# Kernel tuning notes

Measured on AMD Instinct MI355X. Metric: run time of the kernel, lower is better.

Reference implementation:

```python
import jax, jax.numpy as jnp
import numpy as np

WIN_LEN = 400
WIN_INC = 100
FFT_LEN = 512
EPSILON = float(np.finfo(np.float32).eps)


def _make_kernel():
    # periodic (fftbins=True) hamming window, matching scipy.signal.get_window
    n = np.arange(WIN_LEN)
    window = 0.54 - 0.46 * np.cos(2.0 * np.pi * n / WIN_LEN)
    # direct-DFT basis: rfft of identity, truncated to win_len taps
    fourier_basis = np.fft.rfft(np.eye(FFT_LEN))[:WIN_LEN]          # [win_len, fft_len//2+1]
    kernel = np.concatenate([fourier_basis.real, fourier_basis.imag], axis=1).T  # [2*(fft//2+1), win_len]
    kernel = kernel * window                                        # window applied per tap
    return kernel[:, None, :].astype(np.float32)                    # [514, 1, 400] (OIH)


def setup_inputs() -> dict:
    key = jax.random.key(0)
    inputs = jax.random.normal(key, (16, 160000), dtype=jnp.float32)  # [B, L] waveform
    weight = jnp.asarray(_make_kernel())                              # fixed DFT buffer
    return {"inputs": inputs, "weight": weight}


def reference(inputs, weight):
    pad = WIN_LEN - WIN_INC  # 300
    x = inputs[:, None, :]                                   # [B, 1, L]
    x = jnp.pad(x, ((0, 0), (0, 0), (pad, pad)))             # symmetric pad, as in F.pad
    out = jax.lax.conv_general_dilated(
        x, weight,
        window_strides=(WIN_INC,),
        padding='VALID',
        dimension_numbers=('NCH', 'OIH', 'NCH'),
    )                                                        # [B, 514, T]
    r, i = jnp.split(out, 2, axis=1)                         # real / imag halves [B, 257, T]
    mags = jnp.sqrt(jnp.clip(r * r + i * i, EPSILON))
    phase = jnp.arctan2(i + EPSILON, r + EPSILON)
    return mags, phase
```

## Files before the change

### kernel.cpp

```cpp
#include <hip/hip_runtime.h>
#include <math.h>


#define BATCH 16
#define NSAMP 160000
#define NF 257
#define NT 1603
#define KLEN 400
#define INC 100
#define PADL 300
#define EPSF 1.1920928955078125e-7f
#define TAU 1e-2f

#define FPB 16
#define ZSTR 258
#define XSPAN ((FPB - 1) * INC + KLEN)
#define NTB ((NT + FPB - 1) / FPB)

__device__ __forceinline__ float2 cmul(float2 a, float2 b) {
  return make_float2(a.x * b.x - a.y * b.y, a.x * b.y + a.y * b.x);
}

__device__ __forceinline__ void fft16_dif(float2* a) {
  const float C1 = 0.92387953251128674f;
  const float S1 = 0.38268343236508978f;
  const float R2 = 0.70710678118654752f;
  {
    const float2 W[8] = {{1.f, 0.f},  {C1, -S1},  {R2, -R2},  {S1, -C1},
                         {0.f, -1.f}, {-S1, -C1}, {-R2, -R2}, {-C1, -S1}};
    #pragma unroll
    for (int j = 0; j < 8; ++j) {
      float2 u = a[j], v = a[j + 8];
      a[j] = make_float2(u.x + v.x, u.y + v.y);
      float2 d = make_float2(u.x - v.x, u.y - v.y);
      a[j + 8] = cmul(d, W[j]);
    }
  }
  {
    const float2 W[4] = {{1.f, 0.f}, {R2, -R2}, {0.f, -1.f}, {-R2, -R2}};
    #pragma unroll
    for (int h = 0; h < 16; h += 8)
      #pragma unroll
      for (int j = 0; j < 4; ++j) {
        float2 u = a[h + j], v = a[h + j + 4];
        a[h + j] = make_float2(u.x + v.x, u.y + v.y);
        float2 d = make_float2(u.x - v.x, u.y - v.y);
        a[h + j + 4] = cmul(d, W[j]);
      }
  }
  #pragma unroll
  for (int q = 0; q < 16; q += 4) {
    float2 u0 = a[q], v0 = a[q + 2];
    a[q] = make_float2(u0.x + v0.x, u0.y + v0.y);
    a[q + 2] = make_float2(u0.x - v0.x, u0.y - v0.y);
    float2 u1 = a[q + 1], v1 = a[q + 3];
    a[q + 1] = make_float2(u1.x + v1.x, u1.y + v1.y);
    float2 d = make_float2(u1.x - v1.x, u1.y - v1.y);
    a[q + 3] = make_float2(d.y, -d.x);
  }
  #pragma unroll
  for (int q = 0; q < 16; q += 2) {
    float2 u = a[q], v = a[q + 1];
    a[q] = make_float2(u.x + v.x, u.y + v.y);
    a[q + 1] = make_float2(u.x - v.x, u.y - v.y);
  }
}

__device__ __forceinline__ void emit_fp(float rr, float ii, int ff,
                                        const float* __restrict__ w,
                                        const float* xf,
                                        float* __restrict__ out,
                                        long o, long plane) {
  float ie = ii + EPSF, re = rr + EPSF;
  if (fabsf(ie) < TAU && re < TAU) {
    const float* wr = w + (long)ff * KLEN;
    const float* wi = w + (long)(257 + ff) * KLEN;
    float r2 = 0.f, i2 = 0.f;
    for (int k = 0; k < KLEN; ++k) {
      float xv = xf[k];
      r2 = fmaf(wr[k], xv, r2);
      i2 = fmaf(wi[k], xv, i2);
    }
    rr = r2; ii = i2;
  }
  out[o] = sqrtf(fmaxf(rr * rr + ii * ii, EPSF));
  out[o + plane] = atan2f(ii + EPSF, rr + EPSF);
}

__global__ __launch_bounds__(256, 3)
void stft_fft4(const float* __restrict__ x, const float* __restrict__ w,
               float* __restrict__ out) {
  __shared__ float2 Z[FPB * ZSTR];
  __shared__ float2 tw[132];
  __shared__ float2 tw256[256];
  __shared__ __align__(16) float xs[XSPAN];
  __shared__ __align__(16) float win[KLEN];

  const int tid = threadIdx.x;
  const int t0 = blockIdx.x * FPB;
  const int b = blockIdx.y;
  const int tl = tid & 15;
  const int th = tid >> 4;

  const long xb = (long)b * NSAMP;
  const int base = t0 * INC - PADL;
  for (int r = 0; r < 2; ++r) {
    int i4 = r * 256 + tid;
    if (4 * i4 < XSPAN) {
      int g = base + 4 * i4;
      float4 v;
      if (g >= 0 && g + 3 < NSAMP) {
        v = *(const float4*)(x + xb + g);
      } else {
        v.x = (g + 0 >= 0 && g + 0 < NSAMP) ? x[xb + g + 0] : 0.f;
        v.y = (g + 1 >= 0 && g + 1 < NSAMP) ? x[xb + g + 1] : 0.f;
        v.z = (g + 2 >= 0 && g + 2 < NSAMP) ? x[xb + g + 2] : 0.f;
        v.w = (g + 3 >= 0 && g + 3 < NSAMP) ? x[xb + g + 3] : 0.f;
      }
      *(float4*)&xs[4 * i4] = v;
    }
  }
  if (tid < KLEN / 4) {
    *(float4*)&win[4 * tid] = *(const float4*)(w + 4 * tid);
  }
  {
    double a = (double)tid * (6.283185307179586476925286766559 / 256.0);
    tw256[tid] = make_float2((float)cos(a), (float)(-sin(a)));
  }
  if (tid < 132) {
    double a = (double)tid * (6.283185307179586476925286766559 / 512.0);
    tw[tid] = make_float2((float)cos(a), (float)(-sin(a)));
  }
  __syncthreads();

  float2 a[16];
  const float* xf = &xs[tl * INC];
  #pragma unroll
  for (int n1 = 0; n1 < 12; ++n1) {
    int n = 32 * n1 + 2 * th;
    float2 xv = *(const float2*)&xf[n];
    float2 wv = *(const float2*)&win[n];
    a[n1] = make_float2(xv.x * wv.x, xv.y * wv.y);
  }
  {
    int n = 384 + 2 * th;
    if (n < KLEN) {
      float2 xv = *(const float2*)&xf[n];
      float2 wv = *(const float2*)&win[n];
      a[12] = make_float2(xv.x * wv.x, xv.y * wv.y);
    } else {
      a[12] = make_float2(0.f, 0.f);
    }
  }
  a[13] = a[14] = a[15] = make_float2(0.f, 0.f);

  fft16_dif(a);

  static const int BR[16] = {0, 8, 4, 12, 2, 10, 6, 14,
                             1, 9, 5, 13, 3, 11, 7, 15};
  float2* Zf = Z + tl * ZSTR;
  #pragma unroll
  for (int r = 0; r < 16; ++r) {
    const int k1 = BR[r];
    float2 v = (k1 == 0) ? a[r] : cmul(a[r], tw256[th * k1]);
    Zf[th * 16 + k1] = v;
  }
  __syncthreads();

  float2 g[16];
  #pragma unroll
  for (int n2 = 0; n2 < 16; ++n2) g[n2] = Zf[n2 * 16 + th];
  fft16_dif(g);
  #pragma unroll
  for (int r = 0; r < 16; ++r) {
    const int k2 = BR[r];
    Zf[16 * k2 + th] = g[r];
  }
  __syncthreads();

  const long plane = (long)BATCH * NF * NT;
  const long pb = (long)b * NF * NT;
  for (int r = 0; r < 9; ++r) {
    int tau = r * 256 + tid;
    if (tau < FPB * 129) {
      int t = tau & 15;
      int p = tau >> 4;
      float2* Zt = Z + t * ZSTR;
      float2 z0 = Zt[p];
      float2 z1 = Zt[(256 - p) & 255];
      float2 ze = make_float2(0.5f * (z0.x + z1.x), 0.5f * (z0.y - z1.y));
      float2 zo = make_float2(0.5f * (z0.y + z1.y), 0.5f * (z1.x - z0.x));
      float2 T = tw[p];
      float2 tz = cmul(zo, T);
      float2 ya = make_float2(ze.x + tz.x, ze.y + tz.y);
      float2 yb = make_float2(ze.x - tz.x, tz.y - ze.y);
      int tt = t0 + t;
      if (tt < NT) {
        const float* xfr = &xs[t * INC];
        emit_fp(ya.x, ya.y, p, w, xfr, out, pb + (long)p * NT + tt, plane);
        if (p == 0) {
          emit_fp(yb.x, 0.f, 256, w, xfr, out, pb + (long)256 * NT + tt, plane);
        } else {
          emit_fp(yb.x, yb.y, 256 - p, w, xfr, out,
                  pb + (long)(256 - p) * NT + tt, plane);
        }
      }
    }
  }
}

extern "C" void kernel_launch(void* const* d_in, const int* in_sizes, int n_in,
                              void* d_out, int out_size, void* d_ws, size_t ws_size,
                              hipStream_t stream) {
  const float* x = (const float*)d_in[0];
  const float* w = (const float*)d_in[1];
  float* out = (float*)d_out;

  dim3 grid(NTB, BATCH);
  stft_fft4<<<grid, dim3(256), 0, stream>>>(x, w, out);
}
```

Baseline: 156.0 us.

## Halve FFT scratch LDS via two-pass frame processing and use polynomial atan2

Splits the 16 frames per block into two passes of 8, so the shared FFT scratch buffer shrinks by half. This allows the launch bound to rise from 3 to 5 blocks per SM for higher occupancy. It also replaces atan2f with a minimax polynomial built on a hardware reciprocal, which cuts the cost of the phase computation. The trade-offs are more barriers, half the threads idle during each FFT pass, and a small loss of precision in the phase output.

```diff
diff --git a/kernel.cpp b/kernel.cpp
--- a/kernel.cpp
+++ b/kernel.cpp
@@ -64,6 +64,22 @@
     a[q] = make_float2(u.x + v.x, u.y + v.y);
     a[q + 1] = make_float2(u.x - v.x, u.y - v.y);
   }
+}
+
+__device__ __forceinline__ float fast_atan2(float y, float x) {
+  float ax = fabsf(x), ay = fabsf(y);
+  float mx = fmaxf(ax, ay), mn = fminf(ax, ay);
+  float t = mn * __builtin_amdgcn_rcpf(fmaxf(mx, 1e-37f));
+  float s = t * t;
+  float p = fmaf(s, -0.01172120f, 0.05265332f);
+  p = fmaf(s, p, -0.11643287f);
+  p = fmaf(s, p, 0.19354346f);
+  p = fmaf(s, p, -0.33262347f);
+  p = fmaf(s, p, 0.99997726f);
+  float r = t * p;
+  if (ay > ax) r = 1.57079632679489662f - r;
+  if (x < 0.f) r = 3.14159265358979324f - r;
+  return (y < 0.f) ? -r : r;
 }
 
 __device__ __forceinline__ void emit_fp(float rr, float ii, int ff,
@@ -84,13 +100,13 @@
     rr = r2; ii = i2;
   }
   out[o] = sqrtf(fmaxf(rr * rr + ii * ii, EPSF));
-  out[o + plane] = atan2f(ii + EPSF, rr + EPSF);
-}
-
-__global__ __launch_bounds__(256, 3)
-void stft_fft4(const float* __restrict__ x, const float* __restrict__ w,
+  out[o + plane] = fast_atan2(ii + EPSF, rr + EPSF);
+}
+
+__global__ __launch_bounds__(256, 5)
+void stft_fft5(const float* __restrict__ x, const float* __restrict__ w,
                float* __restrict__ out) {
-  __shared__ float2 Z[FPB * ZSTR];
+  __shared__ float2 Z[8 * ZSTR];
   __shared__ float2 tw[132];
   __shared__ float2 tw256[256];
   __shared__ __align__(16) float xs[XSPAN];
@@ -158,54 +174,65 @@
 
   static const int BR[16] = {0, 8, 4, 12, 2, 10, 6, 14,
                              1, 9, 5, 13, 3, 11, 7, 15};
-  float2* Zf = Z + tl * ZSTR;
-  #pragma unroll
-  for (int r = 0; r < 16; ++r) {
-    const int k1 = BR[r];
-    float2 v = (k1 == 0) ? a[r] : cmul(a[r], tw256[th * k1]);
-    Zf[th * 16 + k1] = v;
-  }
-  __syncthreads();
-
-  float2 g[16];
-  #pragma unroll
-  for (int n2 = 0; n2 < 16; ++n2) g[n2] = Zf[n2 * 16 + th];
-  fft16_dif(g);
-  #pragma unroll
-  for (int r = 0; r < 16; ++r) {
-    const int k2 = BR[r];
-    Zf[16 * k2 + th] = g[r];
-  }
-  __syncthreads();
-
   const long plane = (long)BATCH * NF * NT;
   const long pb = (long)b * NF * NT;
-  for (int r = 0; r < 9; ++r) {
-    int tau = r * 256 + tid;
-    if (tau < FPB * 129) {
-      int t = tau & 15;
-      int p = tau >> 4;
-      float2* Zt = Z + t * ZSTR;
-      float2 z0 = Zt[p];
-      float2 z1 = Zt[(256 - p) & 255];
-      float2 ze = make_float2(0.5f * (z0.x + z1.x), 0.5f * (z0.y - z1.y));
-      float2 zo = make_float2(0.5f * (z0.y + z1.y), 0.5f * (z1.x - z0.x));
-      float2 T = tw[p];
-      float2 tz = cmul(zo, T);
-      float2 ya = make_float2(ze.x + tz.x, ze.y + tz.y);
-      float2 yb = make_float2(ze.x - tz.x, tz.y - ze.y);
-      int tt = t0 + t;
-      if (tt < NT) {
-        const float* xfr = &xs[t * INC];
-        emit_fp(ya.x, ya.y, p, w, xfr, out, pb + (long)p * NT + tt, plane);
-        if (p == 0) {
-          emit_fp(yb.x, 0.f, 256, w, xfr, out, pb + (long)256 * NT + tt, plane);
-        } else {
-          emit_fp(yb.x, yb.y, 256 - p, w, xfr, out,
-                  pb + (long)(256 - p) * NT + tt, plane);
+
+  #pragma unroll 1
+  for (int hp = 0; hp < 2; ++hp) {
+    const bool mine = ((tl >> 3) == hp);
+    float2* Zf = Z + (tl & 7) * ZSTR;
+    if (mine) {
+      #pragma unroll
+      for (int r = 0; r < 16; ++r) {
+        const int k1 = BR[r];
+        float2 v = (k1 == 0) ? a[r] : cmul(a[r], tw256[th * k1]);
+        Zf[th * 16 + k1] = v;
+      }
+    }
+    __syncthreads();
+    if (mine) {
+      float2 g[16];
+      #pragma unroll
+      for (int n2 = 0; n2 < 16; ++n2) g[n2] = Zf[n2 * 16 + th];
+      fft16_dif(g);
+      #pragma unroll
+      for (int r = 0; r < 16; ++r) {
+        const int k2 = BR[r];
+        Zf[16 * k2 + th] = g[r];
+      }
+    }
+    __syncthreads();
+
+    for (int r = 0; r < 5; ++r) {
+      int tau = r * 256 + tid;
+      if (tau < 8 * 129) {
+        int t8 = tau & 7;
+        int p = tau >> 3;
+        float2* Zt = Z + t8 * ZSTR;
+        float2 z0 = Zt[p];
+        float2 z1 = Zt[(256 - p) & 255];
+        float2 ze = make_float2(0.5f * (z0.x + z1.x), 0.5f * (z0.y - z1.y));
+        float2 zo = make_float2(0.5f * (z0.y + z1.y), 0.5f * (z1.x - z0.x));
+        float2 T = tw[p];
+        float2 tz = cmul(zo, T);
+        float2 ya = make_float2(ze.x + tz.x, ze.y + tz.y);
+        float2 yb = make_float2(ze.x - tz.x, tz.y - ze.y);
+        int t = hp * 8 + t8;
+        int tt = t0 + t;
+        if (tt < NT) {
+          const float* xfr = &xs[t * INC];
+          emit_fp(ya.x, ya.y, p, w, xfr, out, pb + (long)p * NT + tt, plane);
+          if (p == 0) {
+            emit_fp(yb.x, 0.f, 256, w, xfr, out,
+                    pb + (long)256 * NT + tt, plane);
+          } else {
+            emit_fp(yb.x, yb.y, 256 - p, w, xfr, out,
+                    pb + (long)(256 - p) * NT + tt, plane);
+          }
         }
       }
     }
+    __syncthreads();
   }
 }
 
@@ -217,5 +244,5 @@
   float* out = (float*)d_out;
 
   dim3 grid(NTB, BATCH);
-  stft_fft4<<<grid, dim3(256), 0, stream>>>(x, w, out);
-}
+  stft_fft5<<<grid, dim3(256), 0, stream>>>(x, w, out);
+}
```

New measurement: 270.3 us. 1.73x slower.
